# Kernel tuning notes

Hardware: AMD Instinct MI355X
Metric: run time of the kernel (lower is better)

## Reference

```python
import jax, jax.numpy as jnp
import numpy as np

N_Q = 5000
MEM = 50
KDIM = 50
VDIM = 200
FC = 50
B = 2048
S = 200


def setup_inputs() -> dict:
    key = jax.random.key(0)
    ks = jax.random.split(key, 14)
    inp = {}
    inp["q_data"] = jax.random.randint(ks[0], (B, S), 0, N_Q, dtype=jnp.int64)
    inp["qa_data"] = jax.random.randint(ks[1], (B, S), 0, 2 * N_Q, dtype=jnp.int64)
    # learned parameters (kaiming-ish random init)
    inp["q_embed_w"] = jax.random.normal(ks[2], (N_Q + 1, KDIM), jnp.float32) * 0.2
    inp["qa_embed_w"] = jax.random.normal(ks[3], (2 * N_Q + 1, VDIM), jnp.float32) * 0.1
    inp["key_memory"] = jax.random.normal(ks[4], (MEM, KDIM), jnp.float32) * 0.2
    inp["init_value_memory"] = jax.random.normal(ks[5], (MEM, VDIM), jnp.float32) * 0.1
    # DKVMN write gates: erase (sigmoid) and add (tanh) transforms of qa embedding
    inp["erase_w"] = jax.random.normal(ks[6], (VDIM, VDIM), jnp.float32) * 0.1
    inp["erase_b"] = jnp.zeros((VDIM,), jnp.float32)
    inp["add_w"] = jax.random.normal(ks[7], (VDIM, VDIM), jnp.float32) * 0.1
    inp["add_b"] = jnp.zeros((VDIM,), jnp.float32)
    # prediction MLP: Linear(VDIM+KDIM -> FC), Tanh, Linear(FC -> 1)
    inp["pred_w1"] = jax.random.normal(ks[8], (VDIM + KDIM, FC), jnp.float32) * 0.1
    inp["pred_b1"] = jnp.zeros((FC,), jnp.float32)
    inp["pred_w2"] = jax.random.normal(ks[9], (FC, 1), jnp.float32) * 0.2
    inp["pred_b2"] = jnp.zeros((1,), jnp.float32)
    return inp


def _dkvmn_forward(q_data, qa_data, q_embed_w, qa_embed_w, key_memory,
                   init_value_memory, erase_w, erase_b, add_w, add_b,
                   pred_w1, pred_b1, pred_w2, pred_b2):
    q_emb = q_embed_w[q_data]    # [B, S, KDIM]
    qa_emb = qa_embed_w[qa_data]  # [B, S, VDIM]
    batch = q_data.shape[0]
    Mv0 = jnp.broadcast_to(init_value_memory, (batch, MEM, VDIM))

    def step(Mv, xs):
        q_t, qa_t = xs  # [B, KDIM], [B, VDIM]
        # attention over memory slots
        w = jax.nn.softmax(q_t @ key_memory.T, axis=-1)          # [B, MEM]
        read = jnp.einsum('bm,bmv->bv', w, Mv)                    # [B, VDIM]
        h = jnp.tanh(jnp.concatenate([read, q_t], -1) @ pred_w1 + pred_b1)
        p = jax.nn.sigmoid((h @ pred_w2 + pred_b2)[:, 0])         # [B]
        # erase/add write
        e = jax.nn.sigmoid(qa_t @ erase_w + erase_b)              # [B, VDIM]
        a = jnp.tanh(qa_t @ add_w + add_b)                        # [B, VDIM]
        Mv_new = Mv * (1.0 - w[:, :, None] * e[:, None, :]) + w[:, :, None] * a[:, None, :]
        return Mv_new, p

    xs = (jnp.swapaxes(q_emb, 0, 1), jnp.swapaxes(qa_emb, 0, 1))  # time-major
    _, preds = jax.lax.scan(step, Mv0, xs)                        # [S, B]
    return preds.T                                                # [B, S]


def reference(q_data, qa_data, q_embed_w, qa_embed_w, key_memory,
              init_value_memory, erase_w, erase_b, add_w, add_b,
              pred_w1, pred_b1, pred_w2, pred_b2):
    preds = _dkvmn_forward(q_data, qa_data, q_embed_w, qa_embed_w, key_memory,
                           init_value_memory, erase_w, erase_b, add_w, add_b,
                           pred_w1, pred_b1, pred_w2, pred_b2)
    zeros = jnp.zeros_like(preds)
    return (preds, zeros, zeros, zeros)
```

## Files before the change

### kernel.cpp

```cpp
#include <hip/hip_runtime.h>
#include <hip/hip_fp16.h>


#define NQ1   5001
#define NQA   10001
#define MEMN  50
#define KD    50
#define VD    200
#define FC    50
#define BB    2048
#define SS    200
#define EA_R  16
#define WHS   32

#define EA_B   626
#define WQ_B   1251
#define PACK_B 8
#define PREP_G (EA_B + WQ_B + PACK_B)

typedef unsigned int   u32;
typedef unsigned short u16;
typedef short    s8v __attribute__((ext_vector_type(8)));
typedef float    f4v __attribute__((ext_vector_type(4)));
typedef _Float16 h2v __attribute__((ext_vector_type(2)));
typedef u32      u4v __attribute__((ext_vector_type(4)));

__device__ __forceinline__ float fast_sigmoid(float x) { return 1.f / (1.f + __expf(-x)); }
__device__ __forceinline__ float fast_tanh(float x) {
    float e2 = __expf(2.f * x);
    return 1.f - 2.f / (e2 + 1.f);
}
__device__ __forceinline__ float bfu16_to_f(u16 u) {
    union { float f; u32 i; } x; x.i = ((u32)u) << 16; return x.f;
}
__device__ __forceinline__ u16 f_to_bfu16(float f) {
    union { float f; u32 i; } x; x.f = f;
    return (u16)((x.i + 0x7fffu + ((x.i >> 16) & 1u)) >> 16);
}
__device__ __forceinline__ h2v u32_to_h2v(u32 u) {
    union { u32 i; h2v h; } x; x.i = u; return x.h;
}
__device__ __forceinline__ u16 f16bits(float f) {
    union { __half h; u16 u; } x; x.h = __float2half(f); return x.u;
}
__device__ __forceinline__ float h16_to_f(u16 u) {
    union { u16 u; __half h; } x; x.u = u; return __half2float(x.h);
}

__global__ __launch_bounds__(256) void prep(
        const float* __restrict__ qemb, const float* __restrict__ km,
        const float* __restrict__ w1,   const float* __restrict__ b1,
        const float* __restrict__ qaemb,
        const float* __restrict__ ew,   const float* __restrict__ ebias,
        const float* __restrict__ aw,   const float* __restrict__ abias,
        float* __restrict__ Wt, u32* __restrict__ Wh, float* __restrict__ Q1,
        u32* __restrict__ EA, u16* __restrict__ W1s,
        float* __restrict__ out_aux) {
    const int tid = threadIdx.x;
    const int blk = blockIdx.x;

    for (size_t i = (size_t)blk * 256 + tid; i < 3ull * BB * SS;
         i += (size_t)PREP_G * 256)
        out_aux[i] = 0.f;

    __shared__ float smem[VD * EA_R];

    if (blk < EA_B) {
        const int r0 = blk * EA_R;
        if (tid < VD) {
            #pragma unroll
            for (int r = 0; r < EA_R; ++r) {
                int row = r0 + r;
                smem[tid * EA_R + r] = (row < NQA) ? qaemb[(size_t)row * VD + tid] : 0.f;
            }
        }
        __syncthreads();
        if (tid >= VD) return;

        float accE[EA_R], accA[EA_R];
        #pragma unroll
        for (int r = 0; r < EA_R; ++r) { accE[r] = 0.f; accA[r] = 0.f; }
        for (int k = 0; k < VD; ++k) {
            float we = ew[k * VD + tid];
            float wa = aw[k * VD + tid];
            #pragma unroll
            for (int r = 0; r < EA_R; ++r) {
                float qv = smem[k * EA_R + r];
                accE[r] = fmaf(qv, we, accE[r]);
                accA[r] = fmaf(qv, wa, accA[r]);
            }
        }
        float be = ebias[tid], ba = abias[tid];
        #pragma unroll
        for (int r = 0; r < EA_R; ++r) {
            int row = r0 + r;
            if (row < NQA) {
                u16 ne16 = f16bits(-fast_sigmoid(accE[r] + be));
                u16 a16  = f16bits(fast_tanh(accA[r] + ba));
                EA[(size_t)row * VD + tid] = (u32)ne16 | ((u32)a16 << 16);
            }
        }
    } else if (blk < EA_B + WQ_B) {
        const int lane = tid & 63;
        const int wv   = tid >> 6;
        const int q    = (blk - EA_B) * 4 + wv;
        const bool qok = q < NQ1;
        float* qrow = smem + wv * 64;
        if (qok && lane < KD) qrow[lane] = qemb[q * KD + lane];
        __syncthreads();
        if (!qok) return;

        float s = -1e30f;
        if (lane < MEMN) {
            s = 0.f;
            #pragma unroll
            for (int k = 0; k < KD; ++k) s = fmaf(qrow[k], km[lane * KD + k], s);
        }
        float mx = s;
        #pragma unroll
        for (int off = 32; off >= 1; off >>= 1) mx = fmaxf(mx, __shfl_xor(mx, off, 64));
        float e = (lane < MEMN) ? __expf(s - mx) : 0.f;
        float sum = e;
        #pragma unroll
        for (int off = 32; off >= 1; off >>= 1) sum += __shfl_xor(sum, off, 64);
        float wv_ = (lane < MEMN) ? (e / sum) : 0.f;
        if (lane < MEMN) Wt[q * MEMN + lane] = wv_;

        float plo = __shfl(wv_, 2 * (lane & 31), 64);
        float phi = __shfl(wv_, 2 * (lane & 31) + 1, 64);
        if (lane < 25) {
            Wh[q * WHS + lane] = (u32)f16bits(plo) | ((u32)f16bits(phi) << 16);
        } else if (lane < WHS) {
            Wh[q * WHS + lane] = 0;
        }

        if (lane < FC) {
            float h = b1[lane];
            #pragma unroll
            for (int k = 0; k < KD; ++k)
                h = fmaf(qrow[k], w1[(VD + k) * FC + lane], h);
            Q1[q * FC + lane] = h;
        }
    } else {
        for (int idx = (blk - EA_B - WQ_B) * 256 + tid; idx < 4 * 7 * 64 * 8;
             idx += PACK_B * 256) {
            int j    = idx & 7;
            int lane = (idx >> 3) & 63;
            int kt   = (idx >> 9) % 7;
            int nt   = idx / 3584;
            int k = kt * 32 + ((lane >> 4) << 3) + j;
            int n = nt * 16 + (lane & 15);
            float v = (k < VD && n < FC) ? w1[k * FC + n] : 0.f;
            W1s[idx] = f_to_bfu16(v);
        }
    }
}

__global__ __launch_bounds__(64) void dkvmn_state(
        const int* __restrict__ qd, const int* __restrict__ qad,
        const u32* __restrict__ Wh, const u32* __restrict__ EA,
        const float* __restrict__ ivm, u16* __restrict__ READ) {
    const int tid  = threadIdx.x;
    const int blk  = blockIdx.x;
    const int b    = blk >> 2;
    const int role = blk & 3;
    const int base = b * SS;

    if (role < 3) {
        const int v = role * 64 + tid;

        h2v mv[25];
        #pragma unroll
        for (int i = 0; i < 25; ++i) {
            mv[i].x = (_Float16)ivm[(2 * i) * VD + v];
            mv[i].y = (_Float16)ivm[(2 * i + 1) * VD + v];
        }

        int q_c = __builtin_amdgcn_readfirstlane(qd[base]);
        int q_n = __builtin_amdgcn_readfirstlane(qd[base + 1]);
        int qa0 = __builtin_amdgcn_readfirstlane(qad[base]);
        int qa1 = __builtin_amdgcn_readfirstlane(qad[base + 1]);
        u32 ea_c = EA[(size_t)qa0 * VD + v];
        u32 ea_n = EA[(size_t)qa1 * VD + v];

        for (int t = 0; t < SS; ++t) {
            int tn = t + 2; tn = (tn < SS) ? tn : (SS - 1);
            int q_nn  = __builtin_amdgcn_readfirstlane(qd[base + tn]);
            int qa_nn = __builtin_amdgcn_readfirstlane(qad[base + tn]);
            u32 ea_nn = EA[(size_t)qa_nn * VD + v];

            const u32* wrow = Wh + q_c * WHS;
            h2v nev2 = u32_to_h2v(__builtin_amdgcn_perm(ea_c, ea_c, 0x01000100u));
            h2v av2  = u32_to_h2v(__builtin_amdgcn_perm(ea_c, ea_c, 0x03020302u));

            float rdA = 0.f, rdB = 0.f;
            #pragma unroll
            for (int i = 0; i < 25; i += 2) {
                h2v w0 = u32_to_h2v(wrow[i]);
#if __has_builtin(__builtin_amdgcn_fdot2)
                rdA = __builtin_amdgcn_fdot2(w0, mv[i], rdA, false);
#else
                rdA = fmaf((float)w0.x, (float)mv[i].x,
                      fmaf((float)w0.y, (float)mv[i].y, rdA));
#endif
                mv[i] = __builtin_elementwise_fma(
                    w0, __builtin_elementwise_fma(nev2, mv[i], av2), mv[i]);
                if (i + 1 < 25) {
                    h2v w1p = u32_to_h2v(wrow[i + 1]);
#if __has_builtin(__builtin_amdgcn_fdot2)
                    rdB = __builtin_amdgcn_fdot2(w1p, mv[i + 1], rdB, false);
#else
                    rdB = fmaf((float)w1p.x, (float)mv[i + 1].x,
                          fmaf((float)w1p.y, (float)mv[i + 1].y, rdB));
#endif
                    mv[i + 1] = __builtin_elementwise_fma(
                        w1p, __builtin_elementwise_fma(nev2, mv[i + 1], av2), mv[i + 1]);
                }
            }
            READ[(size_t)(base + t) * VD + v] = f_to_bfu16(rdA + rdB);
            q_c = q_n; q_n = q_nn; ea_c = ea_n; ea_n = ea_nn;
        }
    } else {
        const int v8  = tid & 7;
        const int grp = tid >> 3;
        const int v   = 192 + v8;

        h2v mv4[4];
        #pragma unroll
        for (int j = 0; j < 4; ++j) {
            int p = grp * 4 + j;
            if (p < 25) {
                mv4[j].x = (_Float16)ivm[(2 * p) * VD + v];
                mv4[j].y = (_Float16)ivm[(2 * p + 1) * VD + v];
            } else {
                mv4[j].x = (_Float16)0.f;
                mv4[j].y = (_Float16)0.f;
            }
        }

        int q_c = __builtin_amdgcn_readfirstlane(qd[base]);
        int q_n = __builtin_amdgcn_readfirstlane(qd[base + 1]);
        int qa0 = __builtin_amdgcn_readfirstlane(qad[base]);
        int qa1 = __builtin_amdgcn_readfirstlane(qad[base + 1]);
        u32 ea_c = EA[(size_t)qa0 * VD + v];
        u32 ea_n = EA[(size_t)qa1 * VD + v];
        u4v wq_c = *(const u4v*)(Wh + (size_t)q_c * WHS + grp * 4);
        u4v wq_n = *(const u4v*)(Wh + (size_t)q_n * WHS + grp * 4);

        for (int t = 0; t < SS; ++t) {
            int tn = t + 2; tn = (tn < SS) ? tn : (SS - 1);
            int q_nn  = __builtin_amdgcn_readfirstlane(qd[base + tn]);
            int qa_nn = __builtin_amdgcn_readfirstlane(qad[base + tn]);
            u32 ea_nn = EA[(size_t)qa_nn * VD + v];
            u4v wq_nn = *(const u4v*)(Wh + (size_t)q_nn * WHS + grp * 4);

            h2v nev2 = u32_to_h2v(__builtin_amdgcn_perm(ea_c, ea_c, 0x01000100u));
            h2v av2  = u32_to_h2v(__builtin_amdgcn_perm(ea_c, ea_c, 0x03020302u));

            float rd = 0.f;
            #pragma unroll
            for (int j = 0; j < 4; ++j) {
                h2v w2 = u32_to_h2v(wq_c[j]);
#if __has_builtin(__builtin_amdgcn_fdot2)
                rd = __builtin_amdgcn_fdot2(w2, mv4[j], rd, false);
#else
                rd = fmaf((float)w2.x, (float)mv4[j].x,
                     fmaf((float)w2.y, (float)mv4[j].y, rd));
#endif
                mv4[j] = __builtin_elementwise_fma(
                    w2, __builtin_elementwise_fma(nev2, mv4[j], av2), mv4[j]);
            }
            rd += __shfl_xor(rd, 8, 64);
            rd += __shfl_xor(rd, 16, 64);
            rd += __shfl_xor(rd, 32, 64);
            if (grp == 0)
                READ[(size_t)(base + t) * VD + v] = f_to_bfu16(rd);

            q_c = q_n; q_n = q_nn; ea_c = ea_n; ea_n = ea_nn;
            wq_c = wq_n; wq_n = wq_nn;
        }
    }
}

__global__ __launch_bounds__(256) void mlp_pred(
        const u16* __restrict__ RD, const int* __restrict__ qd,
        const float* __restrict__ Q1tab, const u16* __restrict__ W1s,
        const float* __restrict__ w2, const float* __restrict__ b2,
        float* __restrict__ out) {
    const int tid  = threadIdx.x;
    const int lane = tid & 63;
    const int wv   = tid >> 6;
    const int strip = blockIdx.x * 4 + wv;
    const int row0  = strip * 16;

    const int mrow = lane & 15;
    const int quad = lane >> 4;

    s8v a[7];
    {
        const u16* arow = RD + (size_t)(row0 + mrow) * VD + quad * 8;
        #pragma unroll
        for (int kt = 0; kt < 7; ++kt)
            a[kt] = *(const s8v*)(arow + kt * 32);
    }

    const float b2f = b2[0];
    float pf[4] = {0.f, 0.f, 0.f, 0.f};

    #pragma unroll
    for (int nt = 0; nt < 4; ++nt) {
        s8v bfr[7];
        #pragma unroll
        for (int kt = 0; kt < 7; ++kt)
            bfr[kt] = *(const s8v*)(W1s + (((nt * 7 + kt) * 64) + lane) * 8);

        f4v acc = {0.f, 0.f, 0.f, 0.f};
        #pragma unroll
        for (int kt = 0; kt < 7; ++kt)
            acc = __builtin_amdgcn_mfma_f32_16x16x32_bf16(a[kt], bfr[kt], acc, 0, 0, 0);

        const int f = nt * 16 + mrow;
        const float w2f = (f < FC) ? w2[f] : 0.f;
        #pragma unroll
        for (int r = 0; r < 4; ++r) {
            int row = row0 + quad * 4 + r;
            float h = acc[r] + Q1tab[qd[row] * FC + f];
            pf[r] = fmaf(fast_tanh(h), w2f, pf[r]);
        }
    }

    #pragma unroll
    for (int r = 0; r < 4; ++r) {
        float s = pf[r];
        s += __shfl_xor(s, 1, 64);
        s += __shfl_xor(s, 2, 64);
        s += __shfl_xor(s, 4, 64);
        s += __shfl_xor(s, 8, 64);
        if (mrow == 0)
            out[row0 + quad * 4 + r] = fast_sigmoid(s + b2f);
    }
}

__global__ void dkvmn_main(const int* __restrict__ qd, const int* __restrict__ qad,
                           const float* __restrict__ Wtab, const float* __restrict__ Q1tab,
                           const u32* __restrict__ EA,
                           const float* __restrict__ ivm,
                           const float* __restrict__ w1,
                           const float* __restrict__ w2,
                           const float* __restrict__ b2,
                           float* __restrict__ out) {
    const int tid  = threadIdx.x;
    const int b    = blockIdx.x;
    const int v    = tid;
    const int lane = tid & 63;
    const int wv   = tid >> 6;

    __shared__ alignas(16) float read_lds[4 * 52];
    __shared__ alignas(16) float part_lds[4 * 52];

    float mv[MEMN];
    if (v < VD) {
        #pragma unroll
        for (int m = 0; m < MEMN; ++m) mv[m] = ivm[m * VD + v];
    }
    float w1r[50];
    if (lane < FC) {
        #pragma unroll
        for (int i = 0; i < 50; ++i) w1r[i] = w1[(wv * 50 + i) * FC + lane];
    } else {
        #pragma unroll
        for (int i = 0; i < 50; ++i) w1r[i] = 0.f;
    }
    const float w2f = (tid < FC) ? w2[tid] : 0.f;
    const float b2f = b2[0];

    const int* qrow_i  = qd  + b * SS;
    const int* qarow_i = qad + b * SS;
    const int jchunk = v / 50;
    const int wslot  = jchunk * 52 + (v - jchunk * 50);

    for (int t = 0; t < SS; ++t) {
        const int q  = __builtin_amdgcn_readfirstlane(qrow_i[t]);
        const int qa = __builtin_amdgcn_readfirstlane(qarow_i[t]);
        const float* wrow = Wtab + q * MEMN;

        u32 ea = 0;
        if (v < VD) ea = EA[(size_t)qa * VD + v];
        float ne = h16_to_f((u16)(ea & 0xffffu));
        float av = h16_to_f((u16)(ea >> 16));

        if (v < VD) {
            float rd0 = 0.f, rd1 = 0.f;
            #pragma unroll
            for (int m = 0; m < MEMN; m += 2) {
                float wm0 = wrow[m], wm1 = wrow[m + 1];
                rd0 = fmaf(wm0, mv[m], rd0);
                mv[m] = fmaf(wm0, fmaf(ne, mv[m], av), mv[m]);
                rd1 = fmaf(wm1, mv[m + 1], rd1);
                mv[m + 1] = fmaf(wm1, fmaf(ne, mv[m + 1], av), mv[m + 1]);
            }
            read_lds[wslot] = rd0 + rd1;
        }
        __syncthreads();

        float part = 0.f;
        {
            const float* rlc = read_lds + wv * 52;
            #pragma unroll
            for (int i = 0; i < 48; i += 4) {
                float4 x = *(const float4*)(rlc + i);
                part = fmaf(x.x, w1r[i],     part);
                part = fmaf(x.y, w1r[i + 1], part);
                part = fmaf(x.z, w1r[i + 2], part);
                part = fmaf(x.w, w1r[i + 3], part);
            }
            part = fmaf(rlc[48], w1r[48], part);
            part = fmaf(rlc[49], w1r[49], part);
        }
        if (lane < FC) part_lds[wv * 52 + lane] = part;
        __syncthreads();

        if (wv == 0) {
            float pf = 0.f;
            if (lane < FC) {
                float h = part_lds[lane] + part_lds[52 + lane] +
                          part_lds[104 + lane] + part_lds[156 + lane] +
                          Q1tab[q * FC + lane];
                pf = fast_tanh(h) * w2f;
            }
            #pragma unroll
            for (int off = 32; off >= 1; off >>= 1) pf += __shfl_xor(pf, off, 64);
            if (lane == 0) out[b * SS + t] = fast_sigmoid(pf + b2f);
        }
    }
}

extern "C" void kernel_launch(void* const* d_in, const int* in_sizes, int n_in,
                              void* d_out, int out_size, void* d_ws, size_t ws_size,
                              hipStream_t stream) {
    const int* qd  = (const int*)d_in[0];
    const int* qad = (const int*)d_in[1];
    const float* qemb  = (const float*)d_in[2];
    const float* qaemb = (const float*)d_in[3];
    const float* km    = (const float*)d_in[4];
    const float* ivm   = (const float*)d_in[5];
    const float* ew    = (const float*)d_in[6];
    const float* eb    = (const float*)d_in[7];
    const float* aw    = (const float*)d_in[8];
    const float* ab    = (const float*)d_in[9];
    const float* w1    = (const float*)d_in[10];
    const float* b1    = (const float*)d_in[11];
    const float* w2    = (const float*)d_in[12];
    const float* b2    = (const float*)d_in[13];
    float* out = (float*)d_out;
    (void)in_sizes; (void)n_in; (void)out_size;

    char* ws = (char*)d_ws;
    float* Wt  = (float*)(ws);
    float* Q1  = (float*)(ws + 1000448);
    u32*   EA  = (u32*)  (ws + 2000896);
    u16*   W1s = (u16*)  (ws + 10001920);
    u32*   Wh  = (u32*)  (ws + 10034688);
    u16*   RD  = (u16*)  (ws + 10675200);
    const size_t need = 10675200ull + 163840000ull + 512ull;

    prep<<<PREP_G, 256, 0, stream>>>(qemb, km, w1, b1, qaemb, ew, eb, aw, ab,
                                     Wt, Wh, Q1, EA, W1s, out + (size_t)BB * SS);

    if (ws_size >= need) {
        dkvmn_state<<<BB * 4, 64, 0, stream>>>(qd, qad, Wh, EA, ivm, RD);
        mlp_pred<<<(BB * SS) / 64, 256, 0, stream>>>(RD, qd, Q1, W1s, w2, b2, out);
    } else {
        dkvmn_main<<<BB, 256, 0, stream>>>(qd, qad, Wt, Q1, EA, ivm, w1, w2, b2, out);
    }
}
```

Before: 459.0 us.

## Double-buffer attention weight rows in registers and pack two roles per block

The recurrent state kernel now preloads the next timestep's 25-word attention weight row into a register buffer while computing the current step, alternating between two buffers, instead of loading each weight inside the dependent FMA chain. Blocks now hold two 64-thread waves covering two roles, halving the block count. This is meant to hide global/L2 load latency on the serial time loop, at the cost of about 50 extra VGPRs per thread, which may reduce occupancy.

After: 434.0 us. 1.06x faster.

```diff
diff --git a/kernel.cpp b/kernel.cpp
--- a/kernel.cpp
+++ b/kernel.cpp
@@ -156,18 +156,50 @@
     }
 }
 
-__global__ __launch_bounds__(64) void dkvmn_state(
+__device__ __forceinline__ void state_step(const u32 (&w)[25], u32 ea,
+                                           h2v (&mv)[25], float& rdA, float& rdB) {
+    h2v nev2 = u32_to_h2v(__builtin_amdgcn_perm(ea, ea, 0x01000100u));
+    h2v av2  = u32_to_h2v(__builtin_amdgcn_perm(ea, ea, 0x03020302u));
+    rdA = 0.f; rdB = 0.f;
+    #pragma unroll
+    for (int i = 0; i < 25; i += 2) {
+        h2v w0 = u32_to_h2v(w[i]);
+#if __has_builtin(__builtin_amdgcn_fdot2)
+        rdA = __builtin_amdgcn_fdot2(w0, mv[i], rdA, false);
+#else
+        rdA = fmaf((float)w0.x, (float)mv[i].x,
+              fmaf((float)w0.y, (float)mv[i].y, rdA));
+#endif
+        mv[i] = __builtin_elementwise_fma(
+            w0, __builtin_elementwise_fma(nev2, mv[i], av2), mv[i]);
+        if (i + 1 < 25) {
+            h2v w1p = u32_to_h2v(w[i + 1]);
+#if __has_builtin(__builtin_amdgcn_fdot2)
+            rdB = __builtin_amdgcn_fdot2(w1p, mv[i + 1], rdB, false);
+#else
+            rdB = fmaf((float)w1p.x, (float)mv[i + 1].x,
+                  fmaf((float)w1p.y, (float)mv[i + 1].y, rdB));
+#endif
+            mv[i + 1] = __builtin_elementwise_fma(
+                w1p, __builtin_elementwise_fma(nev2, mv[i + 1], av2), mv[i + 1]);
+        }
+    }
+}
+
+__global__ __launch_bounds__(128) void dkvmn_state(
         const int* __restrict__ qd, const int* __restrict__ qad,
         const u32* __restrict__ Wh, const u32* __restrict__ EA,
         const float* __restrict__ ivm, u16* __restrict__ READ) {
     const int tid  = threadIdx.x;
+    const int lane = tid & 63;
+    const int wid  = tid >> 6;
     const int blk  = blockIdx.x;
-    const int b    = blk >> 2;
-    const int role = blk & 3;
+    const int b    = blk >> 1;
+    const int role = (blk & 1) * 2 + wid;
     const int base = b * SS;
 
     if (role < 3) {
-        const int v = role * 64 + tid;
+        const int v = role * 64 + lane;
 
         h2v mv[25];
         #pragma unroll
@@ -183,46 +215,43 @@
         u32 ea_c = EA[(size_t)qa0 * VD + v];
         u32 ea_n = EA[(size_t)qa1 * VD + v];
 
-        for (int t = 0; t < SS; ++t) {
-            int tn = t + 2; tn = (tn < SS) ? tn : (SS - 1);
-            int q_nn  = __builtin_amdgcn_readfirstlane(qd[base + tn]);
-            int qa_nn = __builtin_amdgcn_readfirstlane(qad[base + tn]);
-            u32 ea_nn = EA[(size_t)qa_nn * VD + v];
-
-            const u32* wrow = Wh + q_c * WHS;
-            h2v nev2 = u32_to_h2v(__builtin_amdgcn_perm(ea_c, ea_c, 0x01000100u));
-            h2v av2  = u32_to_h2v(__builtin_amdgcn_perm(ea_c, ea_c, 0x03020302u));
-
-            float rdA = 0.f, rdB = 0.f;
-            #pragma unroll
-            for (int i = 0; i < 25; i += 2) {
-                h2v w0 = u32_to_h2v(wrow[i]);
-#if __has_builtin(__builtin_amdgcn_fdot2)
-                rdA = __builtin_amdgcn_fdot2(w0, mv[i], rdA, false);
-#else
-                rdA = fmaf((float)w0.x, (float)mv[i].x,
-                      fmaf((float)w0.y, (float)mv[i].y, rdA));
-#endif
-                mv[i] = __builtin_elementwise_fma(
-                    w0, __builtin_elementwise_fma(nev2, mv[i], av2), mv[i]);
-                if (i + 1 < 25) {
-                    h2v w1p = u32_to_h2v(wrow[i + 1]);
-#if __has_builtin(__builtin_amdgcn_fdot2)
-                    rdB = __builtin_amdgcn_fdot2(w1p, mv[i + 1], rdB, false);
-#else
-                    rdB = fmaf((float)w1p.x, (float)mv[i + 1].x,
-                          fmaf((float)w1p.y, (float)mv[i + 1].y, rdB));
-#endif
-                    mv[i + 1] = __builtin_elementwise_fma(
-                        w1p, __builtin_elementwise_fma(nev2, mv[i + 1], av2), mv[i + 1]);
-                }
-            }
-            READ[(size_t)(base + t) * VD + v] = f_to_bfu16(rdA + rdB);
-            q_c = q_n; q_n = q_nn; ea_c = ea_n; ea_n = ea_nn;
+        u32 wb0[25], wb1[25];
+        #pragma unroll
+        for (int i = 0; i < 25; ++i) wb0[i] = Wh[(size_t)q_c * WHS + i];
+
+        for (int t = 0; t < SS; t += 2) {
+            {
+                #pragma unroll
+                for (int i = 0; i < 25; ++i) wb1[i] = Wh[(size_t)q_n * WHS + i];
+
+                int tn = t + 2; tn = (tn < SS) ? tn : (SS - 1);
+                int q_nn  = __builtin_amdgcn_readfirstlane(qd[base + tn]);
+                int qa_nn = __builtin_amdgcn_readfirstlane(qad[base + tn]);
+                u32 ea_nn = EA[(size_t)qa_nn * VD + v];
+
+                float rdA, rdB;
+                state_step(wb0, ea_c, mv, rdA, rdB);
+                READ[(size_t)(base + t) * VD + v] = f_to_bfu16(rdA + rdB);
+                q_c = q_n; q_n = q_nn; ea_c = ea_n; ea_n = ea_nn;
+            }
+            {
+                #pragma unroll
+                for (int i = 0; i < 25; ++i) wb0[i] = Wh[(size_t)q_n * WHS + i];
+
+                int tn = t + 3; tn = (tn < SS) ? tn : (SS - 1);
+                int q_nn  = __builtin_amdgcn_readfirstlane(qd[base + tn]);
+                int qa_nn = __builtin_amdgcn_readfirstlane(qad[base + tn]);
+                u32 ea_nn = EA[(size_t)qa_nn * VD + v];
+
+                float rdA, rdB;
+                state_step(wb1, ea_c, mv, rdA, rdB);
+                READ[(size_t)(base + t + 1) * VD + v] = f_to_bfu16(rdA + rdB);
+                q_c = q_n; q_n = q_nn; ea_c = ea_n; ea_n = ea_nn;
+            }
         }
     } else {
-        const int v8  = tid & 7;
-        const int grp = tid >> 3;
+        const int v8  = lane & 7;
+        const int grp = lane >> 3;
         const int v   = 192 + v8;
 
         h2v mv4[4];
@@ -468,7 +497,7 @@
                                      Wt, Wh, Q1, EA, W1s, out + (size_t)BB * SS);
 
     if (ws_size >= need) {
-        dkvmn_state<<<BB * 4, 64, 0, stream>>>(qd, qad, Wh, EA, ivm, RD);
+        dkvmn_state<<<BB * 2, 128, 0, stream>>>(qd, qad, Wh, EA, ivm, RD);
         mlp_pred<<<(BB * SS) / 64, 256, 0, stream>>>(RD, qd, Q1, W1s, w2, b2, out);
     } else {
         dkvmn_main<<<BB, 256, 0, stream>>>(qd, qad, Wt, Q1, EA, ivm, w1, w2, b2, out);
```
